# Performance work log

Hardware: AMD Instinct MI355X
Metric: run time of the kernel (lower is better)

## Reference

```python
import jax, jax.numpy as jnp
from jax import lax
import numpy as np

B, T, H = 4096, 2048, 32


def setup_inputs() -> dict:
    key = jax.random.key(0)
    ks = jax.random.split(key, 12)
    s = 1.0 / np.sqrt(H)
    u = lambda k, shape: jax.random.uniform(k, shape, jnp.float32, -s, s)
    return {
        "x": jax.random.normal(ks[0], (B, T), jnp.float32),
        "w_ih0": u(ks[1], (H, 1)),
        "w_hh0": u(ks[2], (H, H)),
        "b_ih0": u(ks[3], (H,)),
        "b_hh0": u(ks[4], (H,)),
        "w_ih1": u(ks[5], (H, H)),
        "w_hh1": u(ks[6], (H, H)),
        "b_ih1": u(ks[7], (H,)),
        "b_hh1": u(ks[8], (H,)),
        "w_out": u(ks[9], (1, H)),
        "b_out": u(ks[10], (1,)),
        "future": 0,
    }


def reference(x, w_ih0, w_hh0, b_ih0, b_hh0, w_ih1, w_hh1, b_ih1, b_hh1,
              w_out, b_out, future):
    Bx, Tx = x.shape
    xs = x.T[:, :, None]  # [T, B, 1]
    h0 = jnp.zeros((Bx, H), x.dtype)
    h1 = jnp.zeros((Bx, H), x.dtype)

    def cell(x_t, h0, h1):
        h0 = jnp.tanh(x_t @ w_ih0.T + b_ih0 + h0 @ w_hh0.T + b_hh0)
        h1 = jnp.tanh(h0 @ w_ih1.T + b_ih1 + h1 @ w_hh1.T + b_hh1)
        out = h1 @ w_out.T + b_out  # [B, 1]
        return h0, h1, out

    def step(carry, x_t):
        h0, h1 = carry
        h0, h1, out = cell(x_t, h0, h1)
        return (h0, h1), out

    (h0, h1), outs = lax.scan(step, (h0, h1), xs)  # outs: [T, B, 1]

    if future > 0:
        def fstep(carry, _):
            h0, h1, out = carry
            h0, h1, out = cell(out, h0, h1)
            return (h0, h1, out), out

        _, fouts = lax.scan(fstep, (h0, h1, outs[-1]), None, length=future)
        outs = jnp.concatenate([outs, fouts], axis=0)

    return outs[:, :, 0].T  # [B, T+future]
```

## Files before the change

kernel.cpp:

```cpp
#include <hip/hip_runtime.h>
#include <stdint.h>
#include <math.h>

typedef float f32x4 __attribute__((ext_vector_type(4)));
typedef float f32x2 __attribute__((ext_vector_type(2)));
typedef _Float16 f16x8 __attribute__((ext_vector_type(8)));
typedef _Float16 f16x2 __attribute__((ext_vector_type(2)));

namespace {

constexpr int kB = 4096;
constexpr int kT = 2048;
constexpr int kNSB = kT / 16;
constexpr int kPhases = kT / 4;
constexpr float kS = 2.8853900817779268f;

union Frag { f16x2 h2[4]; f16x8 v; uint32_t u[4]; };
union H2U { f16x2 h; uint32_t u; };

__device__ __forceinline__ f16x2 pk(float a, float b) {
  return __builtin_bit_cast(f16x2, __builtin_amdgcn_cvt_pkrtz(a, b));
}
__device__ __forceinline__ f32x4 mfma(f16x8 a, f16x8 b, f32x4 c) {
  return __builtin_amdgcn_mfma_f32_16x16x32_f16(a, b, c, 0, 0, 0);
}
__device__ __forceinline__ f16x2 fmh(f16x2 a, f16x2 b, f16x2 c) {
  return __builtin_elementwise_fma(a, b, c);
}
__device__ __forceinline__ f16x2 csgn2(f16x2 p, f16x2 s) {
  H2U up, us, r;
  up.h = p; us.h = s;
  r.u = (up.u & 0x7FFF7FFFu) | (us.u & 0x80008000u);
  return r.h;
}

__device__ __forceinline__ void loadfrag_hi(const float* W, int tile, int lane,
                                            Frag& hi) {
  const int mm = lane & 15, gg = lane >> 4;
  const int j = 8 * (mm >> 2) + 4 * tile + (mm & 3);
  const float* p = W + j * 32 + 8 * gg;
  float w8[8];
#pragma unroll
  for (int q = 0; q < 2; ++q) {
    float4 t = ((const float4*)p)[q];
    w8[4 * q + 0] = t.x * kS; w8[4 * q + 1] = t.y * kS;
    w8[4 * q + 2] = t.z * kS; w8[4 * q + 3] = t.w * kS;
  }
#pragma unroll
  for (int q = 0; q < 4; ++q) hi.h2[q] = pk(w8[2 * q], w8[2 * q + 1]);
}

}

extern "C" __global__ __launch_bounds__(128, 1) void rnn2_h16(
    const float* __restrict__ x, const float* __restrict__ w_ih0,
    const float* __restrict__ w_hh0, const float* __restrict__ b_ih0,
    const float* __restrict__ b_hh0, const float* __restrict__ w_ih1,
    const float* __restrict__ w_hh1, const float* __restrict__ b_ih1,
    const float* __restrict__ b_hh1, const float* __restrict__ w_out,
    const float* __restrict__ b_out, float* __restrict__ out,
    float c0, float c1, float c2, float c3, float c4) {
  const int tid = (int)threadIdx.x;
  const int role = tid >> 6;
  const int lane = tid & 63;
  const int g = lane >> 4, m = lane & 15;
  const int rg = (int)blockIdx.x * 16 + m;

  const f16x2 C0 = {(_Float16)c0, (_Float16)c0};
  const f16x2 C1 = {(_Float16)c1, (_Float16)c1};
  const f16x2 C2 = {(_Float16)c2, (_Float16)c2};
  const f16x2 C3 = {(_Float16)c3, (_Float16)c3};
  const f16x2 C4 = {(_Float16)c4, (_Float16)c4};

  __shared__ __align__(16) _Float16 hbuf[8][16][32];
  const int swz = 8 * ((g + (m >> 2)) & 3);

  auto horner2 = [&](f16x2 w) {
    f16x2 p = fmh(w, C4, C3);
    p = fmh(w, p, C2);
    p = fmh(w, p, C1);
    p = fmh(w, p, C0);
    return p;
  };
  auto tanh8 = [&](const f32x4& z0, const f32x4& z1, Frag& hf) {
    float w0 = __builtin_amdgcn_exp2f(-__builtin_fabsf(z0[0]));
    float w1 = __builtin_amdgcn_exp2f(-__builtin_fabsf(z0[1]));
    float w2 = __builtin_amdgcn_exp2f(-__builtin_fabsf(z0[2]));
    float w3 = __builtin_amdgcn_exp2f(-__builtin_fabsf(z0[3]));
    float w4 = __builtin_amdgcn_exp2f(-__builtin_fabsf(z1[0]));
    float w5 = __builtin_amdgcn_exp2f(-__builtin_fabsf(z1[1]));
    float w6 = __builtin_amdgcn_exp2f(-__builtin_fabsf(z1[2]));
    float w7 = __builtin_amdgcn_exp2f(-__builtin_fabsf(z1[3]));
    f16x2 pa = horner2(pk(w0, w1));
    f16x2 pb = horner2(pk(w2, w3));
    f16x2 pc = horner2(pk(w4, w5));
    f16x2 pd = horner2(pk(w6, w7));
    hf.h2[0] = csgn2(pa, pk(z0[0], z0[1]));
    hf.h2[1] = csgn2(pb, pk(z0[2], z0[3]));
    hf.h2[2] = csgn2(pc, pk(z1[0], z1[1]));
    hf.h2[3] = csgn2(pd, pk(z1[2], z1[3]));
  };

  Frag Wa[2], Wb[2];
  f32x4 cv4[2];
  f32x4 wih4[2];
  f16x2 wo2[4];
  float bout = 0.f;
  Frag h0, h1;
#pragma unroll
  for (int q = 0; q < 4; ++q) { h0.u[q] = 0; h1.u[q] = 0; }

  if (role == 0) {
#pragma unroll
    for (int t = 0; t < 2; ++t) loadfrag_hi(w_hh0, t, lane, Wa[t]);
#pragma unroll
    for (int t = 0; t < 2; ++t)
#pragma unroll
      for (int i = 0; i < 4; ++i) {
        int jj = 8 * g + 4 * t + i;
        cv4[t][i] = (b_ih0[jj] + b_hh0[jj]) * kS;
        wih4[t][i] = w_ih0[jj] * kS;
      }
  } else {
#pragma unroll
    for (int t = 0; t < 2; ++t) {
      loadfrag_hi(w_hh1, t, lane, Wa[t]);
      loadfrag_hi(w_ih1, t, lane, Wb[t]);
    }
#pragma unroll
    for (int t = 0; t < 2; ++t)
#pragma unroll
      for (int i = 0; i < 4; ++i) {
        int jj = 8 * g + 4 * t + i;
        cv4[t][i] = (b_ih1[jj] + b_hh1[jj]) * kS;
      }
#pragma unroll
    for (int q = 0; q < 4; ++q) {
      int jj = 8 * g + 4 * (q >> 1) + 2 * (q & 1);
      wo2[q] = pk(w_out[jj], w_out[jj + 1]);
    }
    bout = b_out[0];
  }

  const float* xrow = x + (long)rg * kT;
  float* orow = out + (long)rg * kT;

  auto stepA = [&](float xt, int slot) {
    f32x4 xt4 = {xt, xt, xt, xt};
    f32x4 zi0 = __builtin_elementwise_fma(xt4, wih4[0], cv4[0]);
    f32x4 zi1 = __builtin_elementwise_fma(xt4, wih4[1], cv4[1]);
    f32x4 z0 = mfma(Wa[0].v, h0.v, zi0);
    f32x4 z1 = mfma(Wa[1].v, h0.v, zi1);
    tanh8(z0, z1, h0);
    *reinterpret_cast<f16x8*>(&hbuf[slot][m][swz]) = h0.v;
  };

  float stash[16];
  auto stepB = [&](const Frag& hf, float* st) {
    f32x4 y0 = mfma(Wb[0].v, hf.v, cv4[0]);
    f32x4 y1 = mfma(Wb[1].v, hf.v, cv4[1]);
    y0 = mfma(Wa[0].v, h1.v, y0);
    y1 = mfma(Wa[1].v, h1.v, y1);
    tanh8(y0, y1, h1);
    f16x2 acc = h1.h2[0] * wo2[0];
    acc = fmh(h1.h2[1], wo2[1], acc);
    acc = fmh(h1.h2[2], wo2[2], acc);
    acc = fmh(h1.h2[3], wo2[3], acc);
    *st = (float)acc.x + (float)acc.y;
  };

  auto readslot = [&](int slot) {
    Frag r;
    r.v = *reinterpret_cast<const f16x8*>(&hbuf[slot][m][swz]);
    return r;
  };

  auto reduce_store = [&](int base) {
    float r[16];
#pragma unroll
    for (int i = 0; i < 16; ++i) {
      float s = stash[i];
      s += __shfl_xor(s, 16, 64);
      s += __shfl_xor(s, 32, 64);
      r[i] = s + bout;
    }
    if (lane < 16) {
      float4* dst = (float4*)(orow + base);
      dst[0] = make_float4(r[0], r[1], r[2], r[3]);
      dst[1] = make_float4(r[4], r[5], r[6], r[7]);
      dst[2] = make_float4(r[8], r[9], r[10], r[11]);
      dst[3] = make_float4(r[12], r[13], r[14], r[15]);
    }
  };

  float xc[16], xn[16];
  if (role == 0) {
    float4 q0 = ((const float4*)xrow)[0], q1 = ((const float4*)xrow)[1];
    float4 q2 = ((const float4*)xrow)[2], q3 = ((const float4*)xrow)[3];
    xn[0]=q0.x; xn[1]=q0.y; xn[2]=q0.z; xn[3]=q0.w;
    xn[4]=q1.x; xn[5]=q1.y; xn[6]=q1.z; xn[7]=q1.w;
    xn[8]=q2.x; xn[9]=q2.y; xn[10]=q2.z; xn[11]=q2.w;
    xn[12]=q3.x; xn[13]=q3.y; xn[14]=q3.z; xn[15]=q3.w;
  }

  Frag pf[4];
#pragma unroll
  for (int k = 0; k < 4; ++k)
#pragma unroll
    for (int q = 0; q < 4; ++q) pf[k].u[q] = 0;

  for (int p4 = 0; p4 < kPhases; p4 += 4) {
#pragma unroll
    for (int pp = 0; pp < 4; ++pp) {
      const int p = p4 + pp;
      if (role == 0) {
        if (pp == 0) {
#pragma unroll
          for (int i = 0; i < 16; ++i) xc[i] = xn[i];
          const int nb = ((p4 >> 2) + 1 < kNSB) ? ((p4 >> 2) + 1) : (kNSB - 1);
          const float* src = xrow + nb * 16;
          float4 q0 = ((const float4*)src)[0], q1 = ((const float4*)src)[1];
          float4 q2 = ((const float4*)src)[2], q3 = ((const float4*)src)[3];
          xn[0]=q0.x; xn[1]=q0.y; xn[2]=q0.z; xn[3]=q0.w;
          xn[4]=q1.x; xn[5]=q1.y; xn[6]=q1.z; xn[7]=q1.w;
          xn[8]=q2.x; xn[9]=q2.y; xn[10]=q2.z; xn[11]=q2.w;
          xn[12]=q3.x; xn[13]=q3.y; xn[14]=q3.z; xn[15]=q3.w;
        }
        stepA(xc[4 * pp + 0], (4 * pp + 0) & 7);
        stepA(xc[4 * pp + 1], (4 * pp + 1) & 7);
        stepA(xc[4 * pp + 2], (4 * pp + 2) & 7);
        stepA(xc[4 * pp + 3], (4 * pp + 3) & 7);
      } else {
        if (pp == 1 && p4 >= 4) reduce_store(((p4 - 4) >> 2) * 16);
        if (p >= 1) {
          pf[0] = readslot((4 * pp + 4) & 7);
          pf[1] = readslot((4 * pp + 5) & 7);
          pf[2] = readslot((4 * pp + 6) & 7);
          pf[3] = readslot((4 * pp + 7) & 7);
          stepB(pf[0], &stash[(4 * pp + 12) & 15]);
          stepB(pf[1], &stash[(4 * pp + 13) & 15]);
          stepB(pf[2], &stash[(4 * pp + 14) & 15]);
          stepB(pf[3], &stash[(4 * pp + 15) & 15]);
        }
      }
      asm volatile("s_waitcnt lgkmcnt(0)\n\ts_barrier" ::: "memory");
    }
  }

  if (role == 1) {
    pf[0] = readslot(4); pf[1] = readslot(5);
    pf[2] = readslot(6); pf[3] = readslot(7);
    stepB(pf[0], &stash[12]);
    stepB(pf[1], &stash[13]);
    stepB(pf[2], &stash[14]);
    stepB(pf[3], &stash[15]);
    reduce_store(kT - 16);
  }
}

namespace {
void tanh_poly_coeffs(float* out5) {
  const int N = 64, D = 5;
  double ATA[5][5] = {}, ATf[5] = {};
  for (int i = 0; i < N; ++i) {
    double u = cos(M_PI * (i + 0.5) / N);
    double w = 0.5 * (u + 1.0);
    double f = (1.0 - w) / (1.0 + w);
    double pw[5];
    pw[0] = 1.0;
    for (int k = 1; k < D; ++k) pw[k] = pw[k - 1] * w;
    for (int r = 0; r < D; ++r) {
      ATf[r] += pw[r] * f;
      for (int c = 0; c < D; ++c) ATA[r][c] += pw[r] * pw[c];
    }
  }
  double M[5][6];
  for (int r = 0; r < D; ++r) {
    for (int c = 0; c < D; ++c) M[r][c] = ATA[r][c];
    M[r][D] = ATf[r];
  }
  for (int col = 0; col < D; ++col) {
    int best = col;
    for (int r = col + 1; r < D; ++r)
      if (fabs(M[r][col]) > fabs(M[best][col])) best = r;
    for (int c = col; c <= D; ++c) {
      double t = M[col][c]; M[col][c] = M[best][c]; M[best][c] = t;
    }
    for (int r = col + 1; r < D; ++r) {
      double s = M[r][col] / M[col][col];
      for (int c = col; c <= D; ++c) M[r][c] -= s * M[col][c];
    }
  }
  double xs[5];
  for (int r = D - 1; r >= 0; --r) {
    double s = M[r][D];
    for (int c = r + 1; c < D; ++c) s -= M[r][c] * xs[c];
    xs[r] = s / M[r][r];
  }
  for (int k = 0; k < D; ++k) out5[k] = (float)xs[k];
}
}

extern "C" void kernel_launch(void* const* d_in, const int* in_sizes, int n_in,
                              void* d_out, int out_size, void* d_ws, size_t ws_size,
                              hipStream_t stream) {
  (void)in_sizes; (void)n_in; (void)d_ws; (void)ws_size; (void)out_size;
  const float* xp = (const float*)d_in[0];
  const float* w_ih0 = (const float*)d_in[1];
  const float* w_hh0 = (const float*)d_in[2];
  const float* b_ih0 = (const float*)d_in[3];
  const float* b_hh0 = (const float*)d_in[4];
  const float* w_ih1 = (const float*)d_in[5];
  const float* w_hh1 = (const float*)d_in[6];
  const float* b_ih1 = (const float*)d_in[7];
  const float* b_hh1 = (const float*)d_in[8];
  const float* w_out = (const float*)d_in[9];
  const float* b_out = (const float*)d_in[10];

  float c[5];
  tanh_poly_coeffs(c);

  dim3 grid(kB / 16);
  dim3 block(128);
  hipLaunchKernelGGL(rnn2_h16, grid, block, 0, stream,
                     xp, w_ih0, w_hh0, b_ih0, b_hh0,
                     w_ih1, w_hh1, b_ih1, b_hh1,
                     w_out, b_out, (float*)d_out,
                     c[0], c[1], c[2], c[3], c[4]);
}
```

Before: 358.6 us.

## Widen producer-consumer pipeline to 16 timesteps per barrier phase

The layer-0 wave now runs 16 timesteps per phase into a 32-slot double-buffered LDS ring, and the layer-1 wave consumes the previous 16 slots, instead of 4 steps per barrier with an 8-slot ring. This cuts the number of workgroup barriers by a factor of four and lets the two waves drift further apart. In exchange it uses more LDS and more registers (16 fragments held at once), and the loop is no longer unrolled. Layer-1 work arrives in coarser chunks, so the pipeline takes longer to fill and drain.

```diff
diff --git a/kernel.cpp b/kernel.cpp
--- a/kernel.cpp
+++ b/kernel.cpp
@@ -3,7 +3,6 @@
 #include <math.h>
 
 typedef float f32x4 __attribute__((ext_vector_type(4)));
-typedef float f32x2 __attribute__((ext_vector_type(2)));
 typedef _Float16 f16x8 __attribute__((ext_vector_type(8)));
 typedef _Float16 f16x2 __attribute__((ext_vector_type(2)));
 
@@ -11,8 +10,6 @@
 
 constexpr int kB = 4096;
 constexpr int kT = 2048;
-constexpr int kNSB = kT / 16;
-constexpr int kPhases = kT / 4;
 constexpr float kS = 2.8853900817779268f;
 
 union Frag { f16x2 h2[4]; f16x8 v; uint32_t u[4]; };
@@ -52,7 +49,7 @@
 
 }
 
-extern "C" __global__ __launch_bounds__(128, 1) void rnn2_h16(
+extern "C" __global__ __launch_bounds__(128, 1) void rnn2_p16(
     const float* __restrict__ x, const float* __restrict__ w_ih0,
     const float* __restrict__ w_hh0, const float* __restrict__ b_ih0,
     const float* __restrict__ b_hh0, const float* __restrict__ w_ih1,
@@ -72,7 +69,7 @@
   const f16x2 C3 = {(_Float16)c3, (_Float16)c3};
   const f16x2 C4 = {(_Float16)c4, (_Float16)c4};
 
-  __shared__ __align__(16) _Float16 hbuf[8][16][32];
+  __shared__ __align__(16) _Float16 hbuf[32][16][32];
   const int swz = 8 * ((g + (m >> 2)) & 3);
 
   auto horner2 = [&](f16x2 w) {
@@ -194,68 +191,48 @@
   };
 
   float xc[16], xn[16];
-  if (role == 0) {
-    float4 q0 = ((const float4*)xrow)[0], q1 = ((const float4*)xrow)[1];
-    float4 q2 = ((const float4*)xrow)[2], q3 = ((const float4*)xrow)[3];
-    xn[0]=q0.x; xn[1]=q0.y; xn[2]=q0.z; xn[3]=q0.w;
-    xn[4]=q1.x; xn[5]=q1.y; xn[6]=q1.z; xn[7]=q1.w;
-    xn[8]=q2.x; xn[9]=q2.y; xn[10]=q2.z; xn[11]=q2.w;
-    xn[12]=q3.x; xn[13]=q3.y; xn[14]=q3.z; xn[15]=q3.w;
-  }
-
-  Frag pf[4];
-#pragma unroll
-  for (int k = 0; k < 4; ++k)
+  auto ldx = [&](float* dst, int chunk) {
+    const float4* s = (const float4*)(xrow + chunk * 16);
+    float4 q0 = s[0], q1 = s[1], q2 = s[2], q3 = s[3];
+    dst[0]=q0.x; dst[1]=q0.y; dst[2]=q0.z; dst[3]=q0.w;
+    dst[4]=q1.x; dst[5]=q1.y; dst[6]=q1.z; dst[7]=q1.w;
+    dst[8]=q2.x; dst[9]=q2.y; dst[10]=q2.z; dst[11]=q2.w;
+    dst[12]=q3.x; dst[13]=q3.y; dst[14]=q3.z; dst[15]=q3.w;
+  };
+  if (role == 0) ldx(xn, 0);
+
+  Frag pf[16];
+#pragma unroll
+  for (int k = 0; k < 16; ++k)
 #pragma unroll
     for (int q = 0; q < 4; ++q) pf[k].u[q] = 0;
 
-  for (int p4 = 0; p4 < kPhases; p4 += 4) {
-#pragma unroll
-    for (int pp = 0; pp < 4; ++pp) {
-      const int p = p4 + pp;
-      if (role == 0) {
-        if (pp == 0) {
-#pragma unroll
-          for (int i = 0; i < 16; ++i) xc[i] = xn[i];
-          const int nb = ((p4 >> 2) + 1 < kNSB) ? ((p4 >> 2) + 1) : (kNSB - 1);
-          const float* src = xrow + nb * 16;
-          float4 q0 = ((const float4*)src)[0], q1 = ((const float4*)src)[1];
-          float4 q2 = ((const float4*)src)[2], q3 = ((const float4*)src)[3];
-          xn[0]=q0.x; xn[1]=q0.y; xn[2]=q0.z; xn[3]=q0.w;
-          xn[4]=q1.x; xn[5]=q1.y; xn[6]=q1.z; xn[7]=q1.w;
-          xn[8]=q2.x; xn[9]=q2.y; xn[10]=q2.z; xn[11]=q2.w;
-          xn[12]=q3.x; xn[13]=q3.y; xn[14]=q3.z; xn[15]=q3.w;
-        }
-        stepA(xc[4 * pp + 0], (4 * pp + 0) & 7);
-        stepA(xc[4 * pp + 1], (4 * pp + 1) & 7);
-        stepA(xc[4 * pp + 2], (4 * pp + 2) & 7);
-        stepA(xc[4 * pp + 3], (4 * pp + 3) & 7);
-      } else {
-        if (pp == 1 && p4 >= 4) reduce_store(((p4 - 4) >> 2) * 16);
-        if (p >= 1) {
-          pf[0] = readslot((4 * pp + 4) & 7);
-          pf[1] = readslot((4 * pp + 5) & 7);
-          pf[2] = readslot((4 * pp + 6) & 7);
-          pf[3] = readslot((4 * pp + 7) & 7);
-          stepB(pf[0], &stash[(4 * pp + 12) & 15]);
-          stepB(pf[1], &stash[(4 * pp + 13) & 15]);
-          stepB(pf[2], &stash[(4 * pp + 14) & 15]);
-          stepB(pf[3], &stash[(4 * pp + 15) & 15]);
-        }
+#pragma unroll 1
+  for (int p = 0; p < 129; ++p) {
+    const int half = p & 1;
+    if (role == 0) {
+      if (p < 128) {
+#pragma unroll
+        for (int i = 0; i < 16; ++i) xc[i] = xn[i];
+        ldx(xn, (p + 1 < 128) ? p + 1 : 127);
+        const int wb = half * 16;
+#pragma unroll
+        for (int k = 0; k < 16; ++k) stepA(xc[k], wb + k);
       }
-      asm volatile("s_waitcnt lgkmcnt(0)\n\ts_barrier" ::: "memory");
-    }
-  }
-
-  if (role == 1) {
-    pf[0] = readslot(4); pf[1] = readslot(5);
-    pf[2] = readslot(6); pf[3] = readslot(7);
-    stepB(pf[0], &stash[12]);
-    stepB(pf[1], &stash[13]);
-    stepB(pf[2], &stash[14]);
-    stepB(pf[3], &stash[15]);
-    reduce_store(kT - 16);
-  }
+    } else {
+      if (p >= 2) reduce_store((p - 2) * 16);
+      if (p >= 1) {
+        const int sb = (1 - half) * 16;
+#pragma unroll
+        for (int k = 0; k < 16; ++k) pf[k] = readslot(sb + k);
+#pragma unroll
+        for (int k = 0; k < 16; ++k) stepB(pf[k], &stash[k]);
+      }
+    }
+    asm volatile("s_waitcnt lgkmcnt(0)\n\ts_barrier" ::: "memory");
+  }
+
+  if (role == 1) reduce_store(kT - 16);
 }
 
 namespace {
@@ -322,7 +299,7 @@
 
   dim3 grid(kB / 16);
   dim3 block(128);
-  hipLaunchKernelGGL(rnn2_h16, grid, block, 0, stream,
+  hipLaunchKernelGGL(rnn2_p16, grid, block, 0, stream,
                      xp, w_ih0, w_hh0, b_ih0, b_hh0,
                      w_ih1, w_hh1, b_ih1, b_hh1,
                      w_out, b_out, (float*)d_out,
```

Result: faster. 327.1 us (-8.8%).
